# Kernel tuning notes

Measured on AMD Instinct MI355X. Metric: run time of the kernel, lower is better.

## Reference

```python
import jax, jax.numpy as jnp
import numpy as np

VOCAB = 21128
D_WENLAN = 2048
SENT_LEN = 44  # hard-coded in original forward


def setup_inputs() -> dict:
    key = jax.random.key(0)
    ks = jax.random.split(key, 8)
    B, S, P = 32, 8, 32
    L = S * SENT_LEN  # 352
    concat_output = jax.random.normal(ks[0], (B, S, D_WENLAN), jnp.float32)
    input_ids = jax.random.randint(ks[1], (B, L), 0, VOCAB, jnp.int32)
    topic_ids = jax.random.randint(ks[2], (B, P), 0, VOCAB, jnp.int32)
    tpw_att_mask = jnp.ones((B, P), jnp.int32)
    tpw_type_ids = jnp.zeros((B, P), jnp.int32)
    attention_mask = jnp.ones((B, L), jnp.int32)
    type_ids = jax.random.randint(ks[3], (B, L), 0, 8, jnp.int32)
    token_table = jax.random.normal(ks[4], (VOCAB, D_WENLAN), jnp.float32) * 0.02
    W1 = jax.random.normal(ks[5], (D_WENLAN, 512), jnp.float32) * 0.02
    b1 = jnp.zeros((512,), jnp.float32)
    W2 = jax.random.normal(ks[6], (512, 768), jnp.float32) * 0.02
    b2 = jnp.zeros((768,), jnp.float32)
    return dict(concat_output=concat_output, input_ids=input_ids, topic_ids=topic_ids,
                tpw_att_mask=tpw_att_mask, tpw_type_ids=tpw_type_ids,
                attention_mask=attention_mask, type_ids=type_ids,
                token_table=token_table, W1=W1, b1=b1, W2=W2, b2=b2)


def reference(concat_output, input_ids, topic_ids, tpw_att_mask, tpw_type_ids,
              attention_mask, type_ids, token_table, W1, b1, W2, b2):
    B, S, D = concat_output.shape
    # vectorized replacement of the python double-loop dict lookups:
    topic_emb = token_table[topic_ids]                      # [B,P,2048]
    inp_emb = token_table[input_ids]                        # [B,L,2048]
    # scatter-add: each sentence block of 44 tokens gets its concat_output row added
    inp_emb = inp_emb.reshape(B, S, SENT_LEN, D) + concat_output[:, :, None, :]
    input_embs = jnp.concatenate([topic_emb, inp_emb.reshape(B, S * SENT_LEN, D)], axis=1)
    # projector MLP (Linear -> tanh -> Linear)
    h = jnp.tanh(jnp.einsum('btd,dk->btk', input_embs, W1) + b1)
    gpt_input_embs = jnp.einsum('btk,ke->bte', h, W2) + b2   # [B,P+L,768]
    # auxiliary concatenated tensors fed to gpt2 (is_train=True path)
    labels = jnp.concatenate([topic_ids, input_ids], axis=1)
    full_type_ids = jnp.concatenate([tpw_type_ids, type_ids], axis=1)
    full_att_mask = jnp.concatenate([tpw_att_mask, attention_mask], axis=1)
    return gpt_input_embs, labels, full_type_ids, full_att_mask
```

## Files before the change

kernel.cpp:

```cpp
#include <hip/hip_runtime.h>
#include <math.h>

typedef _Float16 half8 __attribute__((ext_vector_type(8)));
typedef float f32x4 __attribute__((ext_vector_type(4)));

#define BB 32
#define SS 8
#define PP 32
#define SENT 44
#define LL 352
#define TT 384
#define DD 2048
#define H1 512
#define H2 768
#define MM (BB*TT)
#define OUT0 (MM*H2)

#define GLL16(g, l) __builtin_amdgcn_global_load_lds( \
    (const __attribute__((address_space(1))) void*)(g), \
    (__attribute__((address_space(3))) void*)(l), 16, 0, 0)

__global__ __launch_bounds__(256) void gather_kernel(
    const float* __restrict__ token_table,
    const int*   __restrict__ topic_ids,
    const int*   __restrict__ input_ids,
    const float* __restrict__ concat_output,
    _Float16*    __restrict__ A16)
{
    const int m = blockIdx.x;
    const int b = m / TT;
    const int t = m % TT;
    const float* src;
    const float* addp = nullptr;
    if (t < PP) {
        src = token_table + (size_t)topic_ids[b * PP + t] * DD;
    } else {
        int u = t - PP;
        src = token_table + (size_t)input_ids[b * LL + u] * DD;
        addp = concat_output + ((size_t)b * SS + (u / SENT)) * DD;
    }
    _Float16* dst = A16 + (size_t)m * DD;
    const int base = threadIdx.x * 8;
    float4 v0 = *(const float4*)(src + base);
    float4 v1 = *(const float4*)(src + base + 4);
    if (addp) {
        float4 c0 = *(const float4*)(addp + base);
        float4 c1 = *(const float4*)(addp + base + 4);
        v0.x += c0.x; v0.y += c0.y; v0.z += c0.z; v0.w += c0.w;
        v1.x += c1.x; v1.y += c1.y; v1.z += c1.z; v1.w += c1.w;
    }
    half8 h;
    h[0] = (_Float16)v0.x; h[1] = (_Float16)v0.y; h[2] = (_Float16)v0.z; h[3] = (_Float16)v0.w;
    h[4] = (_Float16)v1.x; h[5] = (_Float16)v1.y; h[6] = (_Float16)v1.z; h[7] = (_Float16)v1.w;
    *(half8*)(dst + base) = h;
}

__global__ __launch_bounds__(256) void transpose_f16_kernel(
    const float* __restrict__ src, _Float16* __restrict__ dst, int R, int C)
{
    __shared__ float tile[32][33];
    int c0 = blockIdx.x * 32;
    int r0 = blockIdx.y * 32;
    int tx = threadIdx.x & 31;
    int ty = threadIdx.x >> 5;
    #pragma unroll
    for (int i = 0; i < 4; ++i)
        tile[ty + i*8][tx] = src[(size_t)(r0 + ty + i*8) * C + c0 + tx];
    __syncthreads();
    #pragma unroll
    for (int i = 0; i < 4; ++i)
        dst[(size_t)(c0 + ty + i*8) * R + r0 + tx] = (_Float16)tile[tx][ty + i*8];
}

__global__ __launch_bounds__(256) void gemm1_kernel(
    const _Float16* __restrict__ A16,
    const _Float16* __restrict__ W1T,
    const float*    __restrict__ b1,
    _Float16*       __restrict__ Hout)
{
    const int tid  = threadIdx.x;
    const int wid  = tid >> 6;
    const int lane = tid & 63;

    const int logical = ((blockIdx.x & 7) * 192) + (blockIdx.x >> 3);
    const int bm = logical >> 3;
    const int bn = logical & 7;

    __shared__ _Float16 As[2][64 * 64];
    __shared__ _Float16 Bs[2][64 * 64];

    const int rl = lane >> 3;
    const int cg = lane & 7;
    const _Float16* asrc = A16 + (size_t)(bm * 64 + wid * 16 + rl) * DD
                               + ((cg ^ rl) << 3);
    const _Float16* bsrc = W1T + (size_t)(bn * 64 + wid * 16 + rl) * DD
                               + ((cg ^ rl) << 3);

    #define G1_ISSUE(buf, k0) {                                            \
        _Pragma("unroll")                                                  \
        for (int q = 0; q < 2; ++q) {                                      \
            GLL16(asrc + (size_t)q * 8 * DD + (k0),                        \
                  &As[buf][(wid * 16 + q * 8) * 64]);                      \
            GLL16(bsrc + (size_t)q * 8 * DD + (k0),                        \
                  &Bs[buf][(wid * 16 + q * 8) * 64]);                      \
        }                                                                  \
    }

    const int wrow = (wid >> 1) * 32;
    const int wcol = (wid & 1) * 32;
    const int fr   = lane & 15;
    const int fg   = lane >> 4;

    f32x4 acc[2][2] = {};

    G1_ISSUE(0, 0);

    const int NT = DD / 64;
    for (int t = 0; t < NT; ++t) {
        __syncthreads();
        if (t + 1 < NT) G1_ISSUE((t + 1) & 1, (t + 1) * 64);
        const int cb = t & 1;
        #pragma unroll
        for (int kk = 0; kk < 2; ++kk) {
            half8 af[2], bf[2];
            #pragma unroll
            for (int i = 0; i < 2; ++i) {
                int row = wrow + i * 16 + fr;
                af[i] = *(const half8*)&As[cb][
                    (row * 64 + kk * 32 + fg * 8) ^ ((row & 7) << 3)];
            }
            #pragma unroll
            for (int j = 0; j < 2; ++j) {
                int row = wcol + j * 16 + fr;
                bf[j] = *(const half8*)&Bs[cb][
                    (row * 64 + kk * 32 + fg * 8) ^ ((row & 7) << 3)];
            }
            #pragma unroll
            for (int i = 0; i < 2; ++i)
                #pragma unroll
                for (int j = 0; j < 2; ++j)
                    acc[i][j] = __builtin_amdgcn_mfma_f32_16x16x32_f16(
                        af[i], bf[j], acc[i][j], 0, 0, 0);
        }
    }

    #pragma unroll
    for (int i = 0; i < 2; ++i) {
        #pragma unroll
        for (int j = 0; j < 2; ++j) {
            int col = bn * 64 + wcol + j * 16 + fr;
            float bias = b1[col];
            #pragma unroll
            for (int r = 0; r < 4; ++r) {
                int row = bm * 64 + wrow + i * 16 + fg * 4 + r;
                Hout[(size_t)row * H1 + col] = (_Float16)tanhf(acc[i][j][r] + bias);
            }
        }
    }
    #undef G1_ISSUE
}

__global__ __launch_bounds__(256) void gemm2_kernel(
    const _Float16* __restrict__ Hin,
    const _Float16* __restrict__ W2T,
    const float*    __restrict__ b2,
    float*          __restrict__ out)
{
    const int tid  = threadIdx.x;
    const int wid  = tid >> 6;
    const int lane = tid & 63;

    const int logical = ((blockIdx.x & 7) * 64) + (blockIdx.x >> 3);
    const int bm = logical >> 2;
    const int bn = logical & 3;

    __shared__ _Float16 As[2][96 * 64];
    __shared__ _Float16 Bs[2][192 * 64];

    const int rl = lane >> 3;
    const int cg = lane & 7;
    const _Float16* asrc = Hin + (size_t)(bm * 96 + wid * 24 + rl) * H1
                               + ((cg ^ rl) << 3);
    const _Float16* bsrc = W2T + (size_t)(bn * 192 + wid * 48 + rl) * H1
                               + ((cg ^ rl) << 3);

    #define G2_ISSUE(buf, k0) {                                           \
        _Pragma("unroll")                                                 \
        for (int q = 0; q < 3; ++q)                                       \
            GLL16(asrc + (size_t)q * 8 * H1 + (k0),                       \
                  &As[buf][(wid * 3 + q) * 512]);                         \
        _Pragma("unroll")                                                 \
        for (int q = 0; q < 6; ++q)                                       \
            GLL16(bsrc + (size_t)q * 8 * H1 + (k0),                       \
                  &Bs[buf][(wid * 6 + q) * 512]);                         \
    }

    const int wrow = (wid >> 1) * 48;
    const int wcol = (wid & 1) * 96;
    const int fr   = lane & 15;
    const int fg   = lane >> 4;

    f32x4 acc[3][6] = {};

    G2_ISSUE(0, 0);

    const int NT = H1 / 64;
    for (int t = 0; t < NT; ++t) {
        __syncthreads();
        if (t + 1 < NT) G2_ISSUE((t + 1) & 1, (t + 1) * 64);
        const int cb = t & 1;
        #pragma unroll
        for (int kk = 0; kk < 2; ++kk) {
            half8 af[3], bf[6];
            #pragma unroll
            for (int i = 0; i < 3; ++i) {
                int row = wrow + i * 16 + fr;
                af[i] = *(const half8*)&As[cb][
                    (row * 64 + kk * 32 + fg * 8) ^ ((row & 7) << 3)];
            }
            #pragma unroll
            for (int j = 0; j < 6; ++j) {
                int row = wcol + j * 16 + fr;
                bf[j] = *(const half8*)&Bs[cb][
                    (row * 64 + kk * 32 + fg * 8) ^ ((row & 7) << 3)];
            }
            #pragma unroll
            for (int i = 0; i < 3; ++i)
                #pragma unroll
                for (int j = 0; j < 6; ++j)
                    acc[i][j] = __builtin_amdgcn_mfma_f32_16x16x32_f16(af[i], bf[j], acc[i][j], 0, 0, 0);
        }
    }

    #pragma unroll
    for (int i = 0; i < 3; ++i) {
        #pragma unroll
        for (int j = 0; j < 6; ++j) {
            int col = bn * 192 + wcol + j * 16 + fr;
            float bias = b2[col];
            #pragma unroll
            for (int r = 0; r < 4; ++r) {
                int row = bm * 96 + wrow + i * 16 + fg * 4 + r;
                out[(size_t)row * H2 + col] = acc[i][j][r] + bias;
            }
        }
    }
    #undef G2_ISSUE
}

__global__ __launch_bounds__(256) void aux_kernel(
    const int* __restrict__ topic_ids,
    const int* __restrict__ input_ids,
    const int* __restrict__ tpw_type_ids,
    const int* __restrict__ type_ids,
    const int* __restrict__ tpw_att_mask,
    const int* __restrict__ attention_mask,
    float* __restrict__ out)
{
    int idx = blockIdx.x * 256 + threadIdx.x;
    if (idx >= MM) return;
    int b = idx / TT, t = idx % TT;
    int lab, ty, mk;
    if (t < PP) {
        lab = topic_ids[b * PP + t];
        ty  = tpw_type_ids[b * PP + t];
        mk  = tpw_att_mask[b * PP + t];
    } else {
        int u = t - PP;
        lab = input_ids[b * LL + u];
        ty  = type_ids[b * LL + u];
        mk  = attention_mask[b * LL + u];
    }
    out[OUT0 + idx]          = (float)lab;
    out[OUT0 + MM + idx]     = (float)ty;
    out[OUT0 + 2 * MM + idx] = (float)mk;
}

extern "C" void kernel_launch(void* const* d_in, const int* in_sizes, int n_in,
                              void* d_out, int out_size, void* d_ws, size_t ws_size,
                              hipStream_t stream) {
    const float* concat_output  = (const float*)d_in[0];
    const int*   input_ids      = (const int*)d_in[1];
    const int*   topic_ids      = (const int*)d_in[2];
    const int*   tpw_att_mask   = (const int*)d_in[3];
    const int*   tpw_type_ids   = (const int*)d_in[4];
    const int*   attention_mask = (const int*)d_in[5];
    const int*   type_ids       = (const int*)d_in[6];
    const float* token_table    = (const float*)d_in[7];
    const float* W1             = (const float*)d_in[8];
    const float* b1             = (const float*)d_in[9];
    const float* W2             = (const float*)d_in[10];
    const float* b2             = (const float*)d_in[11];
    float* out = (float*)d_out;

    _Float16* w1t = (_Float16*)d_ws;
    _Float16* w2t = w1t + (size_t)H1 * DD;
    _Float16* Hws = w2t + (size_t)H2 * H1;
    _Float16* A16 = Hws + (size_t)MM * H1;

    transpose_f16_kernel<<<dim3(H1 / 32, DD / 32), 256, 0, stream>>>(W1, w1t, DD, H1);
    transpose_f16_kernel<<<dim3(H2 / 32, H1 / 32), 256, 0, stream>>>(W2, w2t, H1, H2);
    aux_kernel<<<(MM + 255) / 256, 256, 0, stream>>>(
        topic_ids, input_ids, tpw_type_ids, type_ids, tpw_att_mask, attention_mask, out);
    gather_kernel<<<MM, 256, 0, stream>>>(
        token_table, topic_ids, input_ids, concat_output, A16);

    gemm1_kernel<<<(MM / 64) * (H1 / 64), 256, 0, stream>>>(A16, w1t, b1, Hws);
    gemm2_kernel<<<(MM / 96) * (H2 / 192), 256, 0, stream>>>(Hws, w2t, b2, out);
}
```

Measured before the change: 102.1 us.

## Fuse aux outputs into gather kernel and shrink gemm1 K-tile to 32

```diff
diff --git a/kernel.cpp b/kernel.cpp
--- a/kernel.cpp
+++ b/kernel.cpp
@@ -25,19 +25,41 @@
     const int*   __restrict__ topic_ids,
     const int*   __restrict__ input_ids,
     const float* __restrict__ concat_output,
-    _Float16*    __restrict__ A16)
+    const int*   __restrict__ tpw_type_ids,
+    const int*   __restrict__ type_ids,
+    const int*   __restrict__ tpw_att_mask,
+    const int*   __restrict__ attention_mask,
+    _Float16*    __restrict__ A16,
+    float*       __restrict__ out)
 {
     const int m = blockIdx.x;
     const int b = m / TT;
     const int t = m % TT;
     const float* src;
     const float* addp = nullptr;
+    int tok;
     if (t < PP) {
-        src = token_table + (size_t)topic_ids[b * PP + t] * DD;
+        tok = topic_ids[b * PP + t];
+        src = token_table + (size_t)tok * DD;
     } else {
         int u = t - PP;
-        src = token_table + (size_t)input_ids[b * LL + u] * DD;
+        tok = input_ids[b * LL + u];
+        src = token_table + (size_t)tok * DD;
         addp = concat_output + ((size_t)b * SS + (u / SENT)) * DD;
+    }
+    if (threadIdx.x == 0) {
+        int ty, mk;
+        if (t < PP) {
+            ty = tpw_type_ids[b * PP + t];
+            mk = tpw_att_mask[b * PP + t];
+        } else {
+            int u = t - PP;
+            ty = type_ids[b * LL + u];
+            mk = attention_mask[b * LL + u];
+        }
+        out[OUT0 + m]          = (float)tok;
+        out[OUT0 + MM + m]     = (float)ty;
+        out[OUT0 + 2 * MM + m] = (float)mk;
     }
     _Float16* dst = A16 + (size_t)m * DD;
     const int base = threadIdx.x * 8;
@@ -86,24 +108,19 @@
     const int bm = logical >> 3;
     const int bn = logical & 7;
 
-    __shared__ _Float16 As[2][64 * 64];
-    __shared__ _Float16 Bs[2][64 * 64];
-
-    const int rl = lane >> 3;
-    const int cg = lane & 7;
+    __shared__ _Float16 As[2][64 * 32];
+    __shared__ _Float16 Bs[2][64 * 32];
+
+    const int rl = lane >> 2;
+    const int cg = lane & 3;
     const _Float16* asrc = A16 + (size_t)(bm * 64 + wid * 16 + rl) * DD
-                               + ((cg ^ rl) << 3);
+                               + (cg << 3);
     const _Float16* bsrc = W1T + (size_t)(bn * 64 + wid * 16 + rl) * DD
-                               + ((cg ^ rl) << 3);
+                               + (cg << 3);
 
     #define G1_ISSUE(buf, k0) {                                            \
-        _Pragma("unroll")                                                  \
-        for (int q = 0; q < 2; ++q) {                                      \
-            GLL16(asrc + (size_t)q * 8 * DD + (k0),                        \
-                  &As[buf][(wid * 16 + q * 8) * 64]);                      \
-            GLL16(bsrc + (size_t)q * 8 * DD + (k0),                        \
-                  &Bs[buf][(wid * 16 + q * 8) * 64]);                      \
-        }                                                                  \
+        GLL16(asrc + (k0), &As[buf][(wid * 16) * 32]);                     \
+        GLL16(bsrc + (k0), &Bs[buf][(wid * 16) * 32]);                     \
     }
 
     const int wrow = (wid >> 1) * 32;
@@ -115,33 +132,24 @@
 
     G1_ISSUE(0, 0);
 
-    const int NT = DD / 64;
+    const int NT = DD / 32;
     for (int t = 0; t < NT; ++t) {
         __syncthreads();
-        if (t + 1 < NT) G1_ISSUE((t + 1) & 1, (t + 1) * 64);
+        if (t + 1 < NT) G1_ISSUE((t + 1) & 1, (t + 1) * 32);
         const int cb = t & 1;
-        #pragma unroll
-        for (int kk = 0; kk < 2; ++kk) {
-            half8 af[2], bf[2];
-            #pragma unroll
-            for (int i = 0; i < 2; ++i) {
-                int row = wrow + i * 16 + fr;
-                af[i] = *(const half8*)&As[cb][
-                    (row * 64 + kk * 32 + fg * 8) ^ ((row & 7) << 3)];
-            }
-            #pragma unroll
-            for (int j = 0; j < 2; ++j) {
-                int row = wcol + j * 16 + fr;
-                bf[j] = *(const half8*)&Bs[cb][
-                    (row * 64 + kk * 32 + fg * 8) ^ ((row & 7) << 3)];
-            }
-            #pragma unroll
-            for (int i = 0; i < 2; ++i)
-                #pragma unroll
-                for (int j = 0; j < 2; ++j)
-                    acc[i][j] = __builtin_amdgcn_mfma_f32_16x16x32_f16(
-                        af[i], bf[j], acc[i][j], 0, 0, 0);
-        }
+        half8 af[2], bf[2];
+        #pragma unroll
+        for (int i = 0; i < 2; ++i)
+            af[i] = *(const half8*)&As[cb][(wrow + i * 16 + fr) * 32 + fg * 8];
+        #pragma unroll
+        for (int j = 0; j < 2; ++j)
+            bf[j] = *(const half8*)&Bs[cb][(wcol + j * 16 + fr) * 32 + fg * 8];
+        #pragma unroll
+        for (int i = 0; i < 2; ++i)
+            #pragma unroll
+            for (int j = 0; j < 2; ++j)
+                acc[i][j] = __builtin_amdgcn_mfma_f32_16x16x32_f16(
+                    af[i], bf[j], acc[i][j], 0, 0, 0);
     }
 
     #pragma unroll
@@ -246,34 +254,6 @@
         }
     }
     #undef G2_ISSUE
-}
-
-__global__ __launch_bounds__(256) void aux_kernel(
-    const int* __restrict__ topic_ids,
-    const int* __restrict__ input_ids,
-    const int* __restrict__ tpw_type_ids,
-    const int* __restrict__ type_ids,
-    const int* __restrict__ tpw_att_mask,
-    const int* __restrict__ attention_mask,
-    float* __restrict__ out)
-{
-    int idx = blockIdx.x * 256 + threadIdx.x;
-    if (idx >= MM) return;
-    int b = idx / TT, t = idx % TT;
-    int lab, ty, mk;
-    if (t < PP) {
-        lab = topic_ids[b * PP + t];
-        ty  = tpw_type_ids[b * PP + t];
-        mk  = tpw_att_mask[b * PP + t];
-    } else {
-        int u = t - PP;
-        lab = input_ids[b * LL + u];
-        ty  = type_ids[b * LL + u];
-        mk  = attention_mask[b * LL + u];
-    }
-    out[OUT0 + idx]          = (float)lab;
-    out[OUT0 + MM + idx]     = (float)ty;
-    out[OUT0 + 2 * MM + idx] = (float)mk;
 }
 
 extern "C" void kernel_launch(void* const* d_in, const int* in_sizes, int n_in,
@@ -300,10 +280,9 @@
 
     transpose_f16_kernel<<<dim3(H1 / 32, DD / 32), 256, 0, stream>>>(W1, w1t, DD, H1);
     transpose_f16_kernel<<<dim3(H2 / 32, H1 / 32), 256, 0, stream>>>(W2, w2t, H1, H2);
-    aux_kernel<<<(MM + 255) / 256, 256, 0, stream>>>(
-        topic_ids, input_ids, tpw_type_ids, type_ids, tpw_att_mask, attention_mask, out);
     gather_kernel<<<MM, 256, 0, stream>>>(
-        token_table, topic_ids, input_ids, concat_output, A16);
+        token_table, topic_ids, input_ids, concat_output,
+        tpw_type_ids, type_ids, tpw_att_mask, attention_mask, A16, out);
 
     gemm1_kernel<<<(MM / 64) * (H1 / 64), 256, 0, stream>>>(A16, w1t, b1, Hws);
     gemm2_kernel<<<(MM / 96) * (H2 / 192), 256, 0, stream>>>(Hws, w2t, b2, out);
```

New measurement: 103.5 us. Within noise of the previous version (+1.3%).
